# Performance work log

Measured on AMD Instinct MI355X. Metric: run time of the kernel, lower is better.

The kernel has to match this reference:

```python
import jax, jax.numpy as jnp
import numpy as np

D_MODEL = 768
N_HEADS = 12
D_HEAD = D_MODEL // N_HEADS
D_FF = 3072
LN_EPS = 1e-5


def setup_inputs() -> dict:
    key = jax.random.key(0)
    ks = jax.random.split(key, 16)
    B, L = 2, 2048
    s = 0.02
    inp = {
        "x": jax.random.normal(ks[0], (B, L, D_MODEL), jnp.float32),
        "Wq": jax.random.normal(ks[1], (D_MODEL, D_MODEL), jnp.float32) * s,
        "bq": jnp.zeros((D_MODEL,), jnp.float32),
        "Wk": jax.random.normal(ks[2], (D_MODEL, D_MODEL), jnp.float32) * s,
        "bk": jnp.zeros((D_MODEL,), jnp.float32),
        "Wv": jax.random.normal(ks[3], (D_MODEL, D_MODEL), jnp.float32) * s,
        "bv": jnp.zeros((D_MODEL,), jnp.float32),
        "Wo": jax.random.normal(ks[4], (D_MODEL, D_MODEL), jnp.float32) * s,
        "bo": jnp.zeros((D_MODEL,), jnp.float32),
        "g1": jnp.ones((D_MODEL,), jnp.float32),
        "b1": jnp.zeros((D_MODEL,), jnp.float32),
        "g2": jnp.ones((D_MODEL,), jnp.float32),
        "b2": jnp.zeros((D_MODEL,), jnp.float32),
        "W1": jax.random.normal(ks[5], (D_FF, D_MODEL), jnp.float32) * s,
        "c1": jnp.zeros((D_FF,), jnp.float32),
        "W2": jax.random.normal(ks[6], (D_MODEL, D_FF), jnp.float32) * s,
        "c2": jnp.zeros((D_MODEL,), jnp.float32),
        "is_causal": 1,
    }
    return inp


def _layernorm(x, g, b):
    mu = jnp.mean(x, axis=-1, keepdims=True)
    var = jnp.mean(jnp.square(x - mu), axis=-1, keepdims=True)
    return (x - mu) * jax.lax.rsqrt(var + LN_EPS) * g + b


def _mha(xn, Wq, bq, Wk, bk, Wv, bv, Wo, bo, is_causal):
    B, L, D = xn.shape
    q = (xn @ Wq.T + bq).reshape(B, L, N_HEADS, D_HEAD)
    k = (xn @ Wk.T + bk).reshape(B, L, N_HEADS, D_HEAD)
    v = (xn @ Wv.T + bv).reshape(B, L, N_HEADS, D_HEAD)
    scale = D_HEAD ** -0.5
    # [B, H, Lq, Lk] full score matrix (faithful to naive implementation)
    scores = jnp.einsum("bqhd,bkhd->bhqk", q, k) * scale
    if is_causal:
        mask = jnp.triu(jnp.ones((L, L), dtype=bool), k=1)
        scores = jnp.where(mask, -jnp.inf, scores)
    attn = jax.nn.softmax(scores, axis=-1)
    out = jnp.einsum("bhqk,bkhd->bqhd", attn, v).reshape(B, L, D)
    return out @ Wo.T + bo


def reference(x, Wq, bq, Wk, bk, Wv, bv, Wo, bo, g1, b1, g2, b2, W1, c1, W2, c2, is_causal):
    # pre-norm block, dropout=0 (eval)
    normed = _layernorm(x, g1, b1)
    x = x + _mha(normed, Wq, bq, Wk, bk, Wv, bv, Wo, bo, is_causal)
    normed = _layernorm(x, g2, b2)
    h = jax.nn.gelu(normed @ W1.T + c1, approximate=False)
    x = x + (h @ W2.T + c2)
    return x
```

## Files before the change

kernel.cpp:

```cpp
#include <hip/hip_runtime.h>

typedef __attribute__((ext_vector_type(8))) __bf16 bf16x8;
typedef __attribute__((ext_vector_type(4))) __bf16 bf16x4;
typedef __attribute__((ext_vector_type(4))) float f32x4;

#define D_MODEL 768
#define D_FF    3072
#define NT      4096
#define NH      12
#define DH      64
#define LBATCH  2048
#define LDQKV   2304
#define NQT128  16
#define NCHUNK  4

__device__ __forceinline__ f32x4 mfma16(bf16x8 a, bf16x8 b, f32x4 c) {
  return __builtin_amdgcn_mfma_f32_16x16x32_bf16(a, b, c, 0, 0, 0);
}

__device__ __forceinline__ void gl_lds16(const __bf16* g, __bf16* l) {
  __builtin_amdgcn_global_load_lds(
      (const __attribute__((address_space(1))) void*)g,
      (__attribute__((address_space(3))) void*)l, 16, 0, 0);
}

struct ConvArgs {
  const float* src[6];
  __bf16* dst[6];
  int n4[6];
};

__global__ __launch_bounds__(256) void conv_kernel(ConvArgs a) {
  const int m = blockIdx.y;
  const int i = blockIdx.x * 256 + threadIdx.x;
  if (i < a.n4[m]) {
    float4 v = ((const float4*)a.src[m])[i];
    bf16x4 o = {(__bf16)v.x, (__bf16)v.y, (__bf16)v.z, (__bf16)v.w};
    ((bf16x4*)a.dst[m])[i] = o;
  }
}

__global__ __launch_bounds__(256) void ln_kernel(const float* __restrict__ x,
                                                 const float* __restrict__ g,
                                                 const float* __restrict__ b,
                                                 __bf16* __restrict__ out) {
  const int row  = blockIdx.x * 4 + (threadIdx.x >> 6);
  const int lane = threadIdx.x & 63;
  const float4* xr = (const float4*)(x + (size_t)row * D_MODEL + lane * 12);
  float v[12];
  float4 a0 = xr[0], a1 = xr[1], a2 = xr[2];
  v[0] = a0.x; v[1] = a0.y; v[2]  = a0.z; v[3]  = a0.w;
  v[4] = a1.x; v[5] = a1.y; v[6]  = a1.z; v[7]  = a1.w;
  v[8] = a2.x; v[9] = a2.y; v[10] = a2.z; v[11] = a2.w;
  float s = 0.f;
#pragma unroll
  for (int i = 0; i < 12; ++i) s += v[i];
#pragma unroll
  for (int o = 32; o > 0; o >>= 1) s += __shfl_xor(s, o, 64);
  const float mean = s * (1.0f / 768.0f);
  float vs = 0.f;
#pragma unroll
  for (int i = 0; i < 12; ++i) { float d = v[i] - mean; vs += d * d; }
#pragma unroll
  for (int o = 32; o > 0; o >>= 1) vs += __shfl_xor(vs, o, 64);
  const float rstd = rsqrtf(vs * (1.0f / 768.0f) + 1e-5f);
  const int col0 = lane * 12;
#pragma unroll
  for (int i = 0; i < 12; ++i) {
    float gv = g[col0 + i], bv = b[col0 + i];
    out[(size_t)row * D_MODEL + col0 + i] = (__bf16)((v[i] - mean) * rstd * gv + bv);
  }
}

template <int BN, int EPI, typename OutT>
__global__ __launch_bounds__(256) void gemm_bt(const __bf16* __restrict__ A,
                                               const __bf16* __restrict__ W,
                                               const float* __restrict__ bias,
                                               const float* __restrict__ biasK,
                                               const float* __restrict__ biasV,
                                               const float* __restrict__ res,
                                               OutT* __restrict__ C,
                                               int M, int N, int K) {
  constexpr int WN = (BN == 128) ? 2 : 1;
  constexpr int WM = 4 / WN;
  constexpr int MROWS = 128 / WM;
  constexpr int MF = MROWS / 16;
  constexpr int NF = (BN / WN) / 16;
  __shared__ __bf16 As[128 * 64];
  __shared__ __bf16 Bs[BN * 64];
  const int tid = threadIdx.x;
  const int lane = tid & 63, w = tid >> 6;
  const int wr = w / WN, wc = w % WN;
  const int l15 = lane & 15, l4 = lane >> 4;
  const int m0 = blockIdx.y * 128, n0 = blockIdx.x * BN;

  f32x4 acc[MF][NF];
#pragma unroll
  for (int i = 0; i < MF; ++i)
#pragma unroll
    for (int j = 0; j < NF; ++j) acc[i][j] = f32x4{0.f, 0.f, 0.f, 0.f};

  const int srow = tid >> 3;
  const int sblk = tid & 7;

  for (int k0 = 0; k0 < K; k0 += 64) {
    __syncthreads();
#pragma unroll
    for (int i = 0; i < 4; ++i) {
      const int row = i * 32 + srow;
      gl_lds16(A + (size_t)(m0 + row) * K + k0 + ((sblk ^ (row & 7)) << 3),
               &As[(row * 8 + sblk) * 8]);
    }
#pragma unroll
    for (int i = 0; i < BN / 32; ++i) {
      const int row = i * 32 + srow;
      gl_lds16(W + (size_t)(n0 + row) * K + k0 + ((sblk ^ (row & 7)) << 3),
               &Bs[(row * 8 + sblk) * 8]);
    }
    __syncthreads();
#pragma unroll
    for (int kk = 0; kk < 2; ++kk) {
      const int poff = (((kk * 4 + l4) ^ (l15 & 7)) << 3);
      bf16x8 a[MF], bf[NF];
#pragma unroll
      for (int mf = 0; mf < MF; ++mf)
        a[mf] = *(const bf16x8*)(&As[(wr * MROWS + mf * 16 + l15) * 64 + poff]);
#pragma unroll
      for (int nf = 0; nf < NF; ++nf)
        bf[nf] = *(const bf16x8*)(&Bs[(wc * 64 + nf * 16 + l15) * 64 + poff]);
#pragma unroll
      for (int mf = 0; mf < MF; ++mf)
#pragma unroll
        for (int nf = 0; nf < NF; ++nf)
          acc[mf][nf] = mfma16(a[mf], bf[nf], acc[mf][nf]);
    }
  }

#pragma unroll
  for (int mf = 0; mf < MF; ++mf)
#pragma unroll
    for (int nf = 0; nf < NF; ++nf) {
      const int col = n0 + wc * 64 + nf * 16 + l15;
      float bcol;
      if constexpr (EPI == 3)
        bcol = (col < 768) ? bias[col] : (col < 1536 ? biasK[col - 768] : biasV[col - 1536]);
      else
        bcol = bias[col];
#pragma unroll
      for (int r = 0; r < 4; ++r) {
        const int row = m0 + wr * MROWS + mf * 16 + l4 * 4 + r;
        float vv = acc[mf][nf][r] + bcol;
        if constexpr (EPI == 1) vv = 0.5f * vv * (1.0f + erff(vv * 0.70710678118f));
        if constexpr (EPI == 2) vv += res[(size_t)row * N + col];
        C[(size_t)row * N + col] = (OutT)vv;
      }
    }
}

__global__ __launch_bounds__(256) void attn_part(const __bf16* __restrict__ qkv,
                                                 const int* __restrict__ is_causal,
                                                 __bf16* __restrict__ Opn,
                                                 float* __restrict__ Ml) {
  const int qt = blockIdx.x >> 2, ch = blockIdx.x & 3;
  const int h = blockIdx.y, bb = blockIdx.z;
  const int causal = *is_causal;
  const int nkt = causal ? (2 * qt + 2) : 32;
  const int kt0 = ch * 8;
  if (kt0 >= nkt) return;
  const int ktEnd = (kt0 + 8 < nkt) ? (kt0 + 8) : nkt;

  __shared__ __bf16 Ks[2][64 * 64];
  __shared__ __bf16 Vt[2][64 * 72];
  __shared__ __bf16 Ps[128 * 72];
  const int tid = threadIdx.x, lane = tid & 63, w = tid >> 6;
  const int l15 = lane & 15, l4 = lane >> 4, l15b = l15 >> 3;
  const size_t rowbase = (size_t)bb * LBATCH;

  const int sr0 = tid >> 3, sr1 = sr0 + 32, sdb = tid & 7;
  const int kso = ((sdb ^ (sr0 & 7)) << 3);
  const int vc0 = (((sr0 >> 3) ^ sdb) << 3) + (sr0 & 7);
  const int vc1 = (((sr1 >> 3) ^ sdb) << 3) + (sr1 & 7);

  const __bf16* qp0 = qkv + (rowbase + qt * 128 + w * 32 + l15) * LDQKV + h * DH;
  const __bf16* qp1 = qp0 + 16 * LDQKV;
  bf16x8 bqA0 = *(const bf16x8*)(qp0 + l4 * 8);
  bf16x8 bqA1 = *(const bf16x8*)(qp0 + 32 + l4 * 8);
  bf16x8 bqB0 = *(const bf16x8*)(qp1 + l4 * 8);
  bf16x8 bqB1 = *(const bf16x8*)(qp1 + 32 + l4 * 8);

  const __bf16* kvt0 = qkv + (rowbase + kt0 * 64) * LDQKV + h * DH;

  f32x4 oaccA[4], oaccB[4];
#pragma unroll
  for (int df = 0; df < 4; ++df) {
    oaccA[df] = f32x4{0.f, 0.f, 0.f, 0.f};
    oaccB[df] = f32x4{0.f, 0.f, 0.f, 0.f};
  }
  float lrunA = 0.f, lrunB = 0.f;

  {
    gl_lds16(kvt0 + (size_t)sr0 * LDQKV + 768 + kso, &Ks[0][sr0 * 64 + sdb * 8]);
    gl_lds16(kvt0 + (size_t)sr1 * LDQKV + 768 + kso, &Ks[0][sr1 * 64 + sdb * 8]);
    bf16x8 v0 = *(const bf16x8*)(kvt0 + (size_t)sr0 * LDQKV + 1536 + sdb * 8);
    bf16x8 v1 = *(const bf16x8*)(kvt0 + (size_t)sr1 * LDQKV + 1536 + sdb * 8);
#pragma unroll
    for (int j = 0; j < 8; ++j) {
      Vt[0][(sdb * 8 + j) * 72 + vc0] = v0[j];
      Vt[0][(sdb * 8 + j) * 72 + vc1] = v1[j];
    }
  }
  __syncthreads();

  int cur = 0;
  for (int kt = kt0; kt < ktEnd; ++kt, cur ^= 1) {
    const bool pf = (kt + 1 < ktEnd);
    bf16x8 pv0, pv1;
    if (pf) {
      const __bf16* t = kvt0 + (size_t)(kt + 1 - kt0) * 64 * LDQKV;
      gl_lds16(t + (size_t)sr0 * LDQKV + 768 + kso, &Ks[cur ^ 1][sr0 * 64 + sdb * 8]);
      gl_lds16(t + (size_t)sr1 * LDQKV + 768 + kso, &Ks[cur ^ 1][sr1 * 64 + sdb * 8]);
      pv0 = *(const bf16x8*)(t + (size_t)sr0 * LDQKV + 1536 + sdb * 8);
      pv1 = *(const bf16x8*)(t + (size_t)sr1 * LDQKV + 1536 + sdb * 8);
    }

    f32x4 sA[4], sB[4];
    __builtin_amdgcn_s_setprio(1);
#pragma unroll
    for (int nf = 0; nf < 4; ++nf) {
      const int row = nf * 16 + l15;
      bf16x8 ka0 = *(const bf16x8*)(&Ks[cur][row * 64 + ((l4 ^ (l15 & 7)) << 3)]);
      bf16x8 ka1 = *(const bf16x8*)(&Ks[cur][row * 64 + (((4 + l4) ^ (l15 & 7)) << 3)]);
      sA[nf] = mfma16(ka0, bqA0, f32x4{0.f, 0.f, 0.f, 0.f});
      sA[nf] = mfma16(ka1, bqA1, sA[nf]);
      sB[nf] = mfma16(ka0, bqB0, f32x4{0.f, 0.f, 0.f, 0.f});
      sB[nf] = mfma16(ka1, bqB1, sB[nf]);
    }
    __builtin_amdgcn_s_setprio(0);

    float pA[4][4], pB[4][4];
#pragma unroll
    for (int nf = 0; nf < 4; ++nf)
#pragma unroll
      for (int r = 0; r < 4; ++r) {
        pA[nf][r] = sA[nf][r] * 0.125f;
        pB[nf][r] = sB[nf][r] * 0.125f;
      }
    if (causal && (kt * 64 + 63 > qt * 128 + w * 32)) {
      const int qA = qt * 128 + w * 32 + l15;
      const int qB = qA + 16;
#pragma unroll
      for (int nf = 0; nf < 4; ++nf)
#pragma unroll
        for (int r = 0; r < 4; ++r) {
          const int kv = kt * 64 + nf * 16 + l4 * 4 + r;
          if (kv > qA) pA[nf][r] = -__builtin_inff();
          if (kv > qB) pB[nf][r] = -__builtin_inff();
        }
    }
    float sumA = 0.f, sumB = 0.f;
#pragma unroll
    for (int nf = 0; nf < 4; ++nf)
#pragma unroll
      for (int r = 0; r < 4; ++r) {
        float eA = __expf(pA[nf][r]);
        float eB = __expf(pB[nf][r]);
        pA[nf][r] = eA;
        pB[nf][r] = eB;
        sumA += eA;
        sumB += eB;
      }
    sumA += __shfl_xor(sumA, 16, 64);
    sumA += __shfl_xor(sumA, 32, 64);
    sumB += __shfl_xor(sumB, 16, 64);
    sumB += __shfl_xor(sumB, 32, 64);
    lrunA += sumA;
    lrunB += sumB;

#pragma unroll
    for (int nf = 0; nf < 4; ++nf) {
      bf16x4 a = {(__bf16)pA[nf][0], (__bf16)pA[nf][1], (__bf16)pA[nf][2], (__bf16)pA[nf][3]};
      bf16x4 b = {(__bf16)pB[nf][0], (__bf16)pB[nf][1], (__bf16)pB[nf][2], (__bf16)pB[nf][3]};
      *(bf16x4*)(&Ps[(w * 32 + l15) * 72 + nf * 16 + l4 * 4]) = a;
      *(bf16x4*)(&Ps[(w * 32 + 16 + l15) * 72 + nf * 16 + l4 * 4]) = b;
    }

    __builtin_amdgcn_s_setprio(1);
#pragma unroll
    for (int kk = 0; kk < 2; ++kk) {
      bf16x8 pbA = *(const bf16x8*)(&Ps[(w * 32 + l15) * 72 + kk * 32 + l4 * 8]);
      bf16x8 pbB = *(const bf16x8*)(&Ps[(w * 32 + 16 + l15) * 72 + kk * 32 + l4 * 8]);
#pragma unroll
      for (int df = 0; df < 4; ++df) {
        const int d = df * 16 + l15;
        const int pblk = (kk * 4 + l4) ^ (df * 2 + l15b);
        bf16x8 va = *(const bf16x8*)(&Vt[cur][d * 72 + pblk * 8]);
        oaccA[df] = mfma16(va, pbA, oaccA[df]);
        oaccB[df] = mfma16(va, pbB, oaccB[df]);
      }
    }
    __builtin_amdgcn_s_setprio(0);

    if (pf) {
#pragma unroll
      for (int j = 0; j < 8; ++j) {
        Vt[cur ^ 1][(sdb * 8 + j) * 72 + vc0] = pv0[j];
        Vt[cur ^ 1][(sdb * 8 + j) * 72 + vc1] = pv1[j];
      }
    }
    __syncthreads();
  }

  const size_t slot = ((((size_t)bb * NH + h) * NQT128) + qt) * 4 + ch;
  const int qlA = w * 32 + l15, qlB = qlA + 16;
  if (l4 == 0) {
    Ml[slot * 128 + qlA] = lrunA;
    Ml[slot * 128 + qlB] = lrunB;
  }
  const float invA = 1.0f / lrunA, invB = 1.0f / lrunB;
#pragma unroll
  for (int df = 0; df < 4; ++df) {
    bf16x4 oA = {(__bf16)(oaccA[df][0] * invA), (__bf16)(oaccA[df][1] * invA),
                 (__bf16)(oaccA[df][2] * invA), (__bf16)(oaccA[df][3] * invA)};
    bf16x4 oB = {(__bf16)(oaccB[df][0] * invB), (__bf16)(oaccB[df][1] * invB),
                 (__bf16)(oaccB[df][2] * invB), (__bf16)(oaccB[df][3] * invB)};
    *(bf16x4*)(&Opn[slot * 8192 + (size_t)qlA * 64 + df * 16 + l4 * 4]) = oA;
    *(bf16x4*)(&Opn[slot * 8192 + (size_t)qlB * 64 + df * 16 + l4 * 4]) = oB;
  }
}

__global__ __launch_bounds__(256) void attn_comb(const __bf16* __restrict__ Opn,
                                                 const float* __restrict__ Ml,
                                                 const int* __restrict__ is_causal,
                                                 __bf16* __restrict__ out) {
  const int qt = blockIdx.x, h = blockIdx.y, bb = blockIdx.z;
  const int nkt = (*is_causal) ? (2 * qt + 2) : 32;
  const int nc = (nkt + 7) >> 3;
  const int r = threadIdx.x >> 1;
  const int dh = (threadIdx.x & 1) * 32;
  const size_t slot0 = ((((size_t)bb * NH + h) * NQT128) + qt) * 4;

  float lv[4], L = 0.f;
#pragma unroll
  for (int c = 0; c < 4; ++c) {
    lv[c] = (c < nc) ? Ml[(slot0 + c) * 128 + r] : 0.f;
    L += lv[c];
  }
  const float invL = 1.0f / L;
  float o[32];
#pragma unroll
  for (int j = 0; j < 32; ++j) o[j] = 0.f;
#pragma unroll
  for (int c = 0; c < 4; ++c) {
    if (c < nc) {
      const float wv = lv[c] * invL;
      const bf16x8* op = (const bf16x8*)(Opn + (slot0 + c) * 8192 + (size_t)r * 64 + dh);
#pragma unroll
      for (int u = 0; u < 4; ++u) {
        bf16x8 v = op[u];
#pragma unroll
        for (int j = 0; j < 8; ++j) o[u * 8 + j] += wv * (float)v[j];
      }
    }
  }
  __bf16* po = out + ((size_t)bb * LBATCH + qt * 128 + r) * D_MODEL + h * DH + dh;
#pragma unroll
  for (int u = 0; u < 4; ++u) {
    bf16x8 sv;
#pragma unroll
    for (int j = 0; j < 8; ++j) sv[j] = (__bf16)o[u * 8 + j];
    *(bf16x8*)(po + u * 8) = sv;
  }
}

extern "C" void kernel_launch(void* const* d_in, const int* in_sizes, int n_in,
                              void* d_out, int out_size, void* d_ws, size_t ws_size,
                              hipStream_t stream) {
  const float* x  = (const float*)d_in[0];
  const float* Wq = (const float*)d_in[1];
  const float* bq = (const float*)d_in[2];
  const float* Wk = (const float*)d_in[3];
  const float* bk = (const float*)d_in[4];
  const float* Wv = (const float*)d_in[5];
  const float* bv = (const float*)d_in[6];
  const float* Wo = (const float*)d_in[7];
  const float* bo = (const float*)d_in[8];
  const float* g1 = (const float*)d_in[9];
  const float* b1 = (const float*)d_in[10];
  const float* g2 = (const float*)d_in[11];
  const float* b2 = (const float*)d_in[12];
  const float* W1 = (const float*)d_in[13];
  const float* c1 = (const float*)d_in[14];
  const float* W2 = (const float*)d_in[15];
  const float* c2 = (const float*)d_in[16];
  const int* is_causal = (const int*)d_in[17];
  float* out = (float*)d_out;

  char* ws = (char*)d_ws;
  size_t off = 0;
  __bf16* xn   = (__bf16*)(ws + off); off += (size_t)NT * D_MODEL * 2;
  __bf16* qkv  = (__bf16*)(ws + off); off += (size_t)NT * LDQKV * 2;
  __bf16* hb   = (__bf16*)(ws + off); off += (size_t)NT * D_FF * 2;
  float*  x1   = (float*)(ws + off);  off += (size_t)NT * D_MODEL * 4;
  __bf16* Wqkvb = (__bf16*)(ws + off); off += (size_t)3 * D_MODEL * D_MODEL * 2;
  __bf16* Wob  = (__bf16*)(ws + off); off += (size_t)D_MODEL * D_MODEL * 2;
  __bf16* W1b  = (__bf16*)(ws + off); off += (size_t)D_FF * D_MODEL * 2;
  __bf16* W2b  = (__bf16*)(ws + off); off += (size_t)D_MODEL * D_FF * 2;
  __bf16* Opn = hb;
  float*  Ml  = x1;

  ConvArgs ca;
  ca.src[0] = Wq; ca.dst[0] = Wqkvb;                     ca.n4[0] = D_MODEL * D_MODEL / 4;
  ca.src[1] = Wk; ca.dst[1] = Wqkvb + D_MODEL * D_MODEL; ca.n4[1] = D_MODEL * D_MODEL / 4;
  ca.src[2] = Wv; ca.dst[2] = Wqkvb + 2 * D_MODEL * D_MODEL; ca.n4[2] = D_MODEL * D_MODEL / 4;
  ca.src[3] = Wo; ca.dst[3] = Wob;                       ca.n4[3] = D_MODEL * D_MODEL / 4;
  ca.src[4] = W1; ca.dst[4] = W1b;                       ca.n4[4] = D_FF * D_MODEL / 4;
  ca.src[5] = W2; ca.dst[5] = W2b;                       ca.n4[5] = D_MODEL * D_FF / 4;

  dim3 blk(256);
  dim3 gconv((D_FF * D_MODEL / 4 + 255) / 256, 6);

  conv_kernel<<<gconv, blk, 0, stream>>>(ca);
  ln_kernel<<<NT / 4, blk, 0, stream>>>(x, g1, b1, xn);
  gemm_bt<128, 3, __bf16><<<dim3(LDQKV / 128, NT / 128), blk, 0, stream>>>(
      xn, Wqkvb, bq, bk, bv, nullptr, qkv, NT, LDQKV, D_MODEL);
  attn_part<<<dim3(NQT128 * NCHUNK, NH, 2), blk, 0, stream>>>(qkv, is_causal, Opn, Ml);
  attn_comb<<<dim3(NQT128, NH, 2), blk, 0, stream>>>(Opn, Ml, is_causal, xn);
  gemm_bt<64, 2, float><<<dim3(D_MODEL / 64, NT / 128), blk, 0, stream>>>(
      xn, Wob, bo, nullptr, nullptr, x, x1, NT, D_MODEL, D_MODEL);
  ln_kernel<<<NT / 4, blk, 0, stream>>>(x1, g2, b2, xn);
  gemm_bt<128, 1, __bf16><<<dim3(D_FF / 128, NT / 128), blk, 0, stream>>>(
      xn, W1b, c1, nullptr, nullptr, nullptr, hb, NT, D_FF, D_MODEL);
  gemm_bt<64, 2, float><<<dim3(D_MODEL / 64, NT / 128), blk, 0, stream>>>(
      hb, W2b, c2, nullptr, nullptr, x1, out, NT, D_MODEL, D_FF);
}
```

Before: 198.8 us.

## Enlarge attention query tile to 256 rows with 512-thread blocks

The attention partial kernel now handles 256 query rows per block with 8 waves instead of 128 rows with 4. Each K/V tile staged in shared memory is reused by twice as many queries, and each thread loads one K/V row instead of two. The combine kernel is resized to match. In exchange there are half as many blocks, the causal work split gets coarser, shared memory per block grows, and the partial-output buffer layout changes.

```diff
diff --git a/kernel.cpp b/kernel.cpp
--- a/kernel.cpp
+++ b/kernel.cpp
@@ -11,7 +11,7 @@
 #define DH      64
 #define LBATCH  2048
 #define LDQKV   2304
-#define NQT128  16
+#define NQT256  8
 #define NCHUNK  4
 
 __device__ __forceinline__ f32x4 mfma16(bf16x8 a, bf16x8 b, f32x4 c) {
@@ -157,31 +157,30 @@
     }
 }
 
-__global__ __launch_bounds__(256) void attn_part(const __bf16* __restrict__ qkv,
+__global__ __launch_bounds__(512) void attn_part(const __bf16* __restrict__ qkv,
                                                  const int* __restrict__ is_causal,
                                                  __bf16* __restrict__ Opn,
                                                  float* __restrict__ Ml) {
   const int qt = blockIdx.x >> 2, ch = blockIdx.x & 3;
   const int h = blockIdx.y, bb = blockIdx.z;
   const int causal = *is_causal;
-  const int nkt = causal ? (2 * qt + 2) : 32;
+  const int nkt = causal ? (4 * qt + 4) : 32;
   const int kt0 = ch * 8;
   if (kt0 >= nkt) return;
   const int ktEnd = (kt0 + 8 < nkt) ? (kt0 + 8) : nkt;
 
   __shared__ __bf16 Ks[2][64 * 64];
   __shared__ __bf16 Vt[2][64 * 72];
-  __shared__ __bf16 Ps[128 * 72];
+  __shared__ __bf16 Ps[256 * 72];
   const int tid = threadIdx.x, lane = tid & 63, w = tid >> 6;
   const int l15 = lane & 15, l4 = lane >> 4, l15b = l15 >> 3;
   const size_t rowbase = (size_t)bb * LBATCH;
 
-  const int sr0 = tid >> 3, sr1 = sr0 + 32, sdb = tid & 7;
-  const int kso = ((sdb ^ (sr0 & 7)) << 3);
-  const int vc0 = (((sr0 >> 3) ^ sdb) << 3) + (sr0 & 7);
-  const int vc1 = (((sr1 >> 3) ^ sdb) << 3) + (sr1 & 7);
-
-  const __bf16* qp0 = qkv + (rowbase + qt * 128 + w * 32 + l15) * LDQKV + h * DH;
+  const int sr = tid >> 3, sdb = tid & 7;
+  const int kso = ((sdb ^ (sr & 7)) << 3);
+  const int vc = (((sr >> 3) ^ sdb) << 3) + (sr & 7);
+
+  const __bf16* qp0 = qkv + (rowbase + qt * 256 + w * 32 + l15) * LDQKV + h * DH;
   const __bf16* qp1 = qp0 + 16 * LDQKV;
   bf16x8 bqA0 = *(const bf16x8*)(qp0 + l4 * 8);
   bf16x8 bqA1 = *(const bf16x8*)(qp0 + 32 + l4 * 8);
@@ -199,28 +198,21 @@
   float lrunA = 0.f, lrunB = 0.f;
 
   {
-    gl_lds16(kvt0 + (size_t)sr0 * LDQKV + 768 + kso, &Ks[0][sr0 * 64 + sdb * 8]);
-    gl_lds16(kvt0 + (size_t)sr1 * LDQKV + 768 + kso, &Ks[0][sr1 * 64 + sdb * 8]);
-    bf16x8 v0 = *(const bf16x8*)(kvt0 + (size_t)sr0 * LDQKV + 1536 + sdb * 8);
-    bf16x8 v1 = *(const bf16x8*)(kvt0 + (size_t)sr1 * LDQKV + 1536 + sdb * 8);
-#pragma unroll
-    for (int j = 0; j < 8; ++j) {
-      Vt[0][(sdb * 8 + j) * 72 + vc0] = v0[j];
-      Vt[0][(sdb * 8 + j) * 72 + vc1] = v1[j];
-    }
+    gl_lds16(kvt0 + (size_t)sr * LDQKV + 768 + kso, &Ks[0][sr * 64 + sdb * 8]);
+    bf16x8 v0 = *(const bf16x8*)(kvt0 + (size_t)sr * LDQKV + 1536 + sdb * 8);
+#pragma unroll
+    for (int j = 0; j < 8; ++j) Vt[0][(sdb * 8 + j) * 72 + vc] = v0[j];
   }
   __syncthreads();
 
   int cur = 0;
   for (int kt = kt0; kt < ktEnd; ++kt, cur ^= 1) {
     const bool pf = (kt + 1 < ktEnd);
-    bf16x8 pv0, pv1;
+    bf16x8 pv0;
     if (pf) {
       const __bf16* t = kvt0 + (size_t)(kt + 1 - kt0) * 64 * LDQKV;
-      gl_lds16(t + (size_t)sr0 * LDQKV + 768 + kso, &Ks[cur ^ 1][sr0 * 64 + sdb * 8]);
-      gl_lds16(t + (size_t)sr1 * LDQKV + 768 + kso, &Ks[cur ^ 1][sr1 * 64 + sdb * 8]);
-      pv0 = *(const bf16x8*)(t + (size_t)sr0 * LDQKV + 1536 + sdb * 8);
-      pv1 = *(const bf16x8*)(t + (size_t)sr1 * LDQKV + 1536 + sdb * 8);
+      gl_lds16(t + (size_t)sr * LDQKV + 768 + kso, &Ks[cur ^ 1][sr * 64 + sdb * 8]);
+      pv0 = *(const bf16x8*)(t + (size_t)sr * LDQKV + 1536 + sdb * 8);
     }
 
     f32x4 sA[4], sB[4];
@@ -245,8 +237,8 @@
         pA[nf][r] = sA[nf][r] * 0.125f;
         pB[nf][r] = sB[nf][r] * 0.125f;
       }
-    if (causal && (kt * 64 + 63 > qt * 128 + w * 32)) {
-      const int qA = qt * 128 + w * 32 + l15;
+    if (causal && (kt * 64 + 63 > qt * 256 + w * 32)) {
+      const int qA = qt * 256 + w * 32 + l15;
       const int qB = qA + 16;
 #pragma unroll
       for (int nf = 0; nf < 4; ++nf)
@@ -302,19 +294,16 @@
 
     if (pf) {
 #pragma unroll
-      for (int j = 0; j < 8; ++j) {
-        Vt[cur ^ 1][(sdb * 8 + j) * 72 + vc0] = pv0[j];
-        Vt[cur ^ 1][(sdb * 8 + j) * 72 + vc1] = pv1[j];
-      }
+      for (int j = 0; j < 8; ++j) Vt[cur ^ 1][(sdb * 8 + j) * 72 + vc] = pv0[j];
     }
     __syncthreads();
   }
 
-  const size_t slot = ((((size_t)bb * NH + h) * NQT128) + qt) * 4 + ch;
+  const size_t slot = ((((size_t)bb * NH + h) * NQT256) + qt) * 4 + ch;
   const int qlA = w * 32 + l15, qlB = qlA + 16;
   if (l4 == 0) {
-    Ml[slot * 128 + qlA] = lrunA;
-    Ml[slot * 128 + qlB] = lrunB;
+    Ml[slot * 256 + qlA] = lrunA;
+    Ml[slot * 256 + qlB] = lrunB;
   }
   const float invA = 1.0f / lrunA, invB = 1.0f / lrunB;
 #pragma unroll
@@ -323,26 +312,26 @@
                  (__bf16)(oaccA[df][2] * invA), (__bf16)(oaccA[df][3] * invA)};
     bf16x4 oB = {(__bf16)(oaccB[df][0] * invB), (__bf16)(oaccB[df][1] * invB),
                  (__bf16)(oaccB[df][2] * invB), (__bf16)(oaccB[df][3] * invB)};
-    *(bf16x4*)(&Opn[slot * 8192 + (size_t)qlA * 64 + df * 16 + l4 * 4]) = oA;
-    *(bf16x4*)(&Opn[slot * 8192 + (size_t)qlB * 64 + df * 16 + l4 * 4]) = oB;
-  }
-}
-
-__global__ __launch_bounds__(256) void attn_comb(const __bf16* __restrict__ Opn,
+    *(bf16x4*)(&Opn[slot * 16384 + (size_t)qlA * 64 + df * 16 + l4 * 4]) = oA;
+    *(bf16x4*)(&Opn[slot * 16384 + (size_t)qlB * 64 + df * 16 + l4 * 4]) = oB;
+  }
+}
+
+__global__ __launch_bounds__(512) void attn_comb(const __bf16* __restrict__ Opn,
                                                  const float* __restrict__ Ml,
                                                  const int* __restrict__ is_causal,
                                                  __bf16* __restrict__ out) {
   const int qt = blockIdx.x, h = blockIdx.y, bb = blockIdx.z;
-  const int nkt = (*is_causal) ? (2 * qt + 2) : 32;
+  const int nkt = (*is_causal) ? (4 * qt + 4) : 32;
   const int nc = (nkt + 7) >> 3;
   const int r = threadIdx.x >> 1;
   const int dh = (threadIdx.x & 1) * 32;
-  const size_t slot0 = ((((size_t)bb * NH + h) * NQT128) + qt) * 4;
+  const size_t slot0 = ((((size_t)bb * NH + h) * NQT256) + qt) * 4;
 
   float lv[4], L = 0.f;
 #pragma unroll
   for (int c = 0; c < 4; ++c) {
-    lv[c] = (c < nc) ? Ml[(slot0 + c) * 128 + r] : 0.f;
+    lv[c] = (c < nc) ? Ml[(slot0 + c) * 256 + r] : 0.f;
     L += lv[c];
   }
   const float invL = 1.0f / L;
@@ -353,7 +342,7 @@
   for (int c = 0; c < 4; ++c) {
     if (c < nc) {
       const float wv = lv[c] * invL;
-      const bf16x8* op = (const bf16x8*)(Opn + (slot0 + c) * 8192 + (size_t)r * 64 + dh);
+      const bf16x8* op = (const bf16x8*)(Opn + (slot0 + c) * 16384 + (size_t)r * 64 + dh);
 #pragma unroll
       for (int u = 0; u < 4; ++u) {
         bf16x8 v = op[u];
@@ -362,7 +351,7 @@
       }
     }
   }
-  __bf16* po = out + ((size_t)bb * LBATCH + qt * 128 + r) * D_MODEL + h * DH + dh;
+  __bf16* po = out + ((size_t)bb * LBATCH + qt * 256 + r) * D_MODEL + h * DH + dh;
 #pragma unroll
   for (int u = 0; u < 4; ++u) {
     bf16x8 sv;
@@ -423,8 +412,8 @@
   ln_kernel<<<NT / 4, blk, 0, stream>>>(x, g1, b1, xn);
   gemm_bt<128, 3, __bf16><<<dim3(LDQKV / 128, NT / 128), blk, 0, stream>>>(
       xn, Wqkvb, bq, bk, bv, nullptr, qkv, NT, LDQKV, D_MODEL);
-  attn_part<<<dim3(NQT128 * NCHUNK, NH, 2), blk, 0, stream>>>(qkv, is_causal, Opn, Ml);
-  attn_comb<<<dim3(NQT128, NH, 2), blk, 0, stream>>>(Opn, Ml, is_causal, xn);
+  attn_part<<<dim3(NQT256 * NCHUNK, NH, 2), dim3(512), 0, stream>>>(qkv, is_causal, Opn, Ml);
+  attn_comb<<<dim3(NQT256, NH, 2), dim3(512), 0, stream>>>(Opn, Ml, is_causal, xn);
   gemm_bt<64, 2, float><<<dim3(D_MODEL / 64, NT / 128), blk, 0, stream>>>(
       xn, Wob, bo, nullptr, nullptr, x, x1, NT, D_MODEL, D_MODEL);
   ln_kernel<<<NT / 4, blk, 0, stream>>>(x1, g2, b2, xn);
```

New measurement: 200.9 us. No clear change (+1.1%).

## Double-buffer GEMM LDS tiles with async prefetch two stages ahead

Applied to the files above, without the earlier changes.

Converts the bf16 GEMM main loop to double-buffered LDS tiles. Global-to-LDS loads for tile k+2 are issued while tile k is computed, and partial vmcnt waits let outstanding loads overlap the MFMA work. This targets the load latency that was exposed between the two __syncthreads per K step. In exchange it doubles shared memory use, which may reduce occupancy, and it relies on hand-coded waitcnt counts matching the number of issued loads.

```diff
diff --git a/kernel.cpp b/kernel.cpp
--- a/kernel.cpp
+++ b/kernel.cpp
@@ -86,8 +86,8 @@
   constexpr int MROWS = 128 / WM;
   constexpr int MF = MROWS / 16;
   constexpr int NF = (BN / WN) / 16;
-  __shared__ __bf16 As[128 * 64];
-  __shared__ __bf16 Bs[BN * 64];
+  __shared__ __bf16 As[2][128 * 64];
+  __shared__ __bf16 Bs[2][BN * 64];
   const int tid = threadIdx.x;
   const int lane = tid & 63, w = tid >> 6;
   const int wr = w / WN, wc = w % WN;
@@ -103,37 +103,53 @@
   const int srow = tid >> 3;
   const int sblk = tid & 7;
 
-  for (int k0 = 0; k0 < K; k0 += 64) {
-    __syncthreads();
+  auto STAGE = [&](int buf, int k0) {
 #pragma unroll
     for (int i = 0; i < 4; ++i) {
       const int row = i * 32 + srow;
       gl_lds16(A + (size_t)(m0 + row) * K + k0 + ((sblk ^ (row & 7)) << 3),
-               &As[(row * 8 + sblk) * 8]);
+               &As[buf][(row * 8 + sblk) * 8]);
     }
 #pragma unroll
     for (int i = 0; i < BN / 32; ++i) {
       const int row = i * 32 + srow;
       gl_lds16(W + (size_t)(n0 + row) * K + k0 + ((sblk ^ (row & 7)) << 3),
-               &Bs[(row * 8 + sblk) * 8]);
-    }
-    __syncthreads();
+               &Bs[buf][(row * 8 + sblk) * 8]);
+    }
+  };
+
+  const int NKI = K >> 6;
+  STAGE(0, 0);
+  STAGE(1, 64);
+
+  for (int k = 0; k < NKI; ++k) {
+    if (k + 1 < NKI) {
+      if constexpr (BN == 128)
+        asm volatile("s_waitcnt vmcnt(8)\ns_barrier" ::: "memory");
+      else
+        asm volatile("s_waitcnt vmcnt(6)\ns_barrier" ::: "memory");
+    } else {
+      asm volatile("s_waitcnt vmcnt(0)\ns_barrier" ::: "memory");
+    }
+    const int buf = k & 1;
 #pragma unroll
     for (int kk = 0; kk < 2; ++kk) {
       const int poff = (((kk * 4 + l4) ^ (l15 & 7)) << 3);
       bf16x8 a[MF], bf[NF];
 #pragma unroll
       for (int mf = 0; mf < MF; ++mf)
-        a[mf] = *(const bf16x8*)(&As[(wr * MROWS + mf * 16 + l15) * 64 + poff]);
+        a[mf] = *(const bf16x8*)(&As[buf][(wr * MROWS + mf * 16 + l15) * 64 + poff]);
 #pragma unroll
       for (int nf = 0; nf < NF; ++nf)
-        bf[nf] = *(const bf16x8*)(&Bs[(wc * 64 + nf * 16 + l15) * 64 + poff]);
+        bf[nf] = *(const bf16x8*)(&Bs[buf][(wc * 64 + nf * 16 + l15) * 64 + poff]);
 #pragma unroll
       for (int mf = 0; mf < MF; ++mf)
 #pragma unroll
         for (int nf = 0; nf < NF; ++nf)
           acc[mf][nf] = mfma16(a[mf], bf[nf], acc[mf][nf]);
     }
+    asm volatile("s_waitcnt lgkmcnt(0)\ns_barrier" ::: "memory");
+    if (k + 2 < NKI) STAGE(buf, (k + 2) << 6);
   }
 
 #pragma unroll
```

New measurement: 213.5 us. 1.07x slower.

## Split-K the W2 down-projection GEMM with a separate combine kernel

Applied to the files above, without the earlier changes.

The final FFN GEMM (K=3072) is split into two K halves launched as a z-dimension of the grid, doubling block count from 384 to 768 to better fill the GPU. Each half writes bf16 partials into the reused qkv buffer, and a new elementwise kernel sums the partials, adds bias and residual, and writes the fp32 output. This adds an extra kernel launch and partial-sum traffic, and rounding partials to bf16 loses some precision.

```diff
diff --git a/kernel.cpp b/kernel.cpp
--- a/kernel.cpp
+++ b/kernel.cpp
@@ -80,7 +80,7 @@
                                                const float* __restrict__ biasV,
                                                const float* __restrict__ res,
                                                OutT* __restrict__ C,
-                                               int M, int N, int K) {
+                                               int M, int N, int K, int kSplit) {
   constexpr int WN = (BN == 128) ? 2 : 1;
   constexpr int WM = 4 / WN;
   constexpr int MROWS = 128 / WM;
@@ -93,6 +93,7 @@
   const int wr = w / WN, wc = w % WN;
   const int l15 = lane & 15, l4 = lane >> 4;
   const int m0 = blockIdx.y * 128, n0 = blockIdx.x * BN;
+  const int kBeg = blockIdx.z * kSplit;
 
   f32x4 acc[MF][NF];
 #pragma unroll
@@ -103,7 +104,7 @@
   const int srow = tid >> 3;
   const int sblk = tid & 7;
 
-  for (int k0 = 0; k0 < K; k0 += 64) {
+  for (int k0 = kBeg; k0 < kBeg + kSplit; k0 += 64) {
     __syncthreads();
 #pragma unroll
     for (int i = 0; i < 4; ++i) {
@@ -135,6 +136,9 @@
           acc[mf][nf] = mfma16(a[mf], bf[nf], acc[mf][nf]);
     }
   }
+
+  OutT* Cz = C;
+  if constexpr (EPI == 4) Cz = C + (size_t)blockIdx.z * M * N;
 
 #pragma unroll
   for (int mf = 0; mf < MF; ++mf)
@@ -144,6 +148,8 @@
       float bcol;
       if constexpr (EPI == 3)
         bcol = (col < 768) ? bias[col] : (col < 1536 ? biasK[col - 768] : biasV[col - 1536]);
+      else if constexpr (EPI == 4)
+        bcol = 0.f;
       else
         bcol = bias[col];
 #pragma unroll
@@ -152,9 +158,27 @@
         float vv = acc[mf][nf][r] + bcol;
         if constexpr (EPI == 1) vv = 0.5f * vv * (1.0f + erff(vv * 0.70710678118f));
         if constexpr (EPI == 2) vv += res[(size_t)row * N + col];
-        C[(size_t)row * N + col] = (OutT)vv;
-      }
-    }
+        Cz[(size_t)row * N + col] = (OutT)vv;
+      }
+    }
+}
+
+__global__ __launch_bounds__(256) void w2_comb(const __bf16* __restrict__ P,
+                                               const float* __restrict__ bias,
+                                               const float* __restrict__ res,
+                                               float* __restrict__ out) {
+  const size_t i = (size_t)blockIdx.x * 256 + threadIdx.x;
+  const size_t e = i * 4;
+  bf16x4 p0 = *(const bf16x4*)(P + e);
+  bf16x4 p1 = *(const bf16x4*)(P + (size_t)NT * D_MODEL + e);
+  const int col = (int)(e % D_MODEL);
+  float4 r4 = *(const float4*)(res + e);
+  float4 o;
+  o.x = (float)p0[0] + (float)p1[0] + bias[col + 0] + r4.x;
+  o.y = (float)p0[1] + (float)p1[1] + bias[col + 1] + r4.y;
+  o.z = (float)p0[2] + (float)p1[2] + bias[col + 2] + r4.z;
+  o.w = (float)p0[3] + (float)p1[3] + bias[col + 3] + r4.w;
+  *(float4*)(out + e) = o;
 }
 
 __global__ __launch_bounds__(256) void attn_part(const __bf16* __restrict__ qkv,
@@ -407,6 +431,7 @@
   __bf16* W2b  = (__bf16*)(ws + off); off += (size_t)D_MODEL * D_FF * 2;
   __bf16* Opn = hb;
   float*  Ml  = x1;
+  __bf16* Pk = qkv;
 
   ConvArgs ca;
   ca.src[0] = Wq; ca.dst[0] = Wqkvb;                     ca.n4[0] = D_MODEL * D_MODEL / 4;
@@ -422,14 +447,15 @@
   conv_kernel<<<gconv, blk, 0, stream>>>(ca);
   ln_kernel<<<NT / 4, blk, 0, stream>>>(x, g1, b1, xn);
   gemm_bt<128, 3, __bf16><<<dim3(LDQKV / 128, NT / 128), blk, 0, stream>>>(
-      xn, Wqkvb, bq, bk, bv, nullptr, qkv, NT, LDQKV, D_MODEL);
+      xn, Wqkvb, bq, bk, bv, nullptr, qkv, NT, LDQKV, D_MODEL, D_MODEL);
   attn_part<<<dim3(NQT128 * NCHUNK, NH, 2), blk, 0, stream>>>(qkv, is_causal, Opn, Ml);
   attn_comb<<<dim3(NQT128, NH, 2), blk, 0, stream>>>(Opn, Ml, is_causal, xn);
   gemm_bt<64, 2, float><<<dim3(D_MODEL / 64, NT / 128), blk, 0, stream>>>(
-      xn, Wob, bo, nullptr, nullptr, x, x1, NT, D_MODEL, D_MODEL);
+      xn, Wob, bo, nullptr, nullptr, x, x1, NT, D_MODEL, D_MODEL, D_MODEL);
   ln_kernel<<<NT / 4, blk, 0, stream>>>(x1, g2, b2, xn);
   gemm_bt<128, 1, __bf16><<<dim3(D_FF / 128, NT / 128), blk, 0, stream>>>(
-      xn, W1b, c1, nullptr, nullptr, nullptr, hb, NT, D_FF, D_MODEL);
-  gemm_bt<64, 2, float><<<dim3(D_MODEL / 64, NT / 128), blk, 0, stream>>>(
-      hb, W2b, c2, nullptr, nullptr, x1, out, NT, D_MODEL, D_FF);
-}
+      xn, W1b, c1, nullptr, nullptr, nullptr, hb, NT, D_FF, D_MODEL, D_MODEL);
+  gemm_bt<64, 4, __bf16><<<dim3(D_MODEL / 64, NT / 128, 2), blk, 0, stream>>>(
+      hb, W2b, nullptr, nullptr, nullptr, nullptr, Pk, NT, D_MODEL, D_FF, D_FF / 2);
+  w2_comb<<<NT * D_MODEL / 4 / 256, blk, 0, stream>>>(Pk, c2, x1, out);
+}
```

Measured after the change: 194.8 us (median of 2 runs). -2.0%, faster.
